# Kernel optimization log

Hardware: AMD Instinct MI355X
Metric: run time of the kernel (lower is better)

## Reference

```python
import jax, jax.numpy as jnp
import numpy as np

B, T, D, HS = 8, 2048, 1024, 64

def setup_inputs() -> dict:
    key = jax.random.key(0)
    ks = jax.random.split(key, 7)
    s = 1.0 / np.sqrt(D)
    return {
        "x": jax.random.normal(ks[0], (B, T, D), dtype=jnp.float32),
        "wq_w": jax.random.normal(ks[1], (HS, D), dtype=jnp.float32) * s,
        "wq_b": jax.random.normal(ks[2], (HS,), dtype=jnp.float32) * 0.01,
        "wk_w": jax.random.normal(ks[3], (HS, D), dtype=jnp.float32) * s,
        "wk_b": jax.random.normal(ks[4], (HS,), dtype=jnp.float32) * 0.01,
        "wv_w": jax.random.normal(ks[5], (HS, D), dtype=jnp.float32) * s,
        "wv_b": jax.random.normal(ks[6], (HS,), dtype=jnp.float32) * 0.01,
    }

def reference(x, wq_w, wq_b, wk_w, wk_b, wv_w, wv_b):
    Tq = x.shape[1]
    q = jnp.einsum('btd,hd->bth', x, wq_w) + wq_b  # [B,T,HS]
    k = jnp.einsum('btd,hd->bth', x, wk_w) + wk_b
    v = jnp.einsum('btd,hd->bth', x, wv_w) + wv_b
    scores = jnp.einsum('bth,bsh->bts', q, k) / jnp.sqrt(jnp.float32(HS))  # [B,T,T]
    causal = jnp.tril(jnp.ones((Tq, Tq), dtype=bool))
    scores = jnp.where(causal, scores, -jnp.inf)
    weight = jax.nn.softmax(scores, axis=-1)
    # dropout p=0.0 -> identity
    out = jnp.einsum('bts,bsh->bth', weight, v)  # [B,T,HS]
    return out
```

## Files before the change

### kernel.cpp

```cpp
#include <hip/hip_runtime.h>

#define DD 1024
#define HSZ 64
#define TT 2048
#define NB 8
#define MM (NB*TT)
#define PART_STRIDE 1040

typedef unsigned short U16;
typedef U16 u16x4 __attribute__((ext_vector_type(4)));
typedef U16 u16x8 __attribute__((ext_vector_type(8)));
typedef float f32x4 __attribute__((ext_vector_type(4)));

__device__ inline U16 f2b(float f) {
    unsigned u = __builtin_bit_cast(unsigned, f);
    u += 0x7FFFu + ((u >> 16) & 1u);
    return (U16)(u >> 16);
}

__device__ inline f32x4 mfma16(u16x8 a, u16x8 b, f32x4 c) {
    return __builtin_amdgcn_mfma_f32_16x16x32_bf16(a, b, c, 0, 0, 0);
}

__device__ inline void gld16(const void* g, void* l) {
    __builtin_amdgcn_global_load_lds(
        (const __attribute__((address_space(1))) void*)g,
        (__attribute__((address_space(3))) void*)l, 16, 0, 0);
}

__global__ __launch_bounds__(256) void wconv_kernel(
    const float* __restrict__ wq, const float* __restrict__ wk,
    const float* __restrict__ wv, U16* __restrict__ wb)
{
    int t = blockIdx.x * 256 + threadIdx.x;
    int n = t >> 8;
    int k0 = (t & 255) * 4;
    const float* src = n < 64 ? wq + (size_t)n * DD
                     : (n < 128 ? wk + (size_t)(n - 64) * DD
                                : wv + (size_t)(n - 128) * DD);
    float4 v = *(const float4*)(src + k0);
    int chunk = k0 >> 6, kc = k0 & 63;
    int byte = (n * 128 + kc * 2) ^ ((n & 7) << 4);
    u16x4 h = { f2b(v.x), f2b(v.y), f2b(v.z), f2b(v.w) };
    *(u16x4*)((char*)wb + (size_t)chunk * 24576 + byte) = h;
}

__global__ __launch_bounds__(512) void qkv_kernel(
    const float* __restrict__ x, const U16* __restrict__ wb,
    const float* __restrict__ wqb, const float* __restrict__ wkb, const float* __restrict__ wvb,
    U16* __restrict__ qb, U16* __restrict__ kb, U16* __restrict__ vt)
{
    __shared__ __attribute__((aligned(16))) U16 Bs[2][12288];
    __shared__ __attribute__((aligned(16))) U16 As[2][2048];

    const int tid = threadIdx.x, lane = tid & 63, w = tid >> 6;
    const int wm = w >> 2, wn = w & 3, g = lane >> 4, c = lane & 15;
    const int m0 = blockIdx.x * 32;

    const int arow = tid >> 4, aseg = tid & 15;
    const float* axp = x + (size_t)(m0 + arow) * DD + aseg * 4;
    const int abyte = (arow * 128 + aseg * 8) ^ ((arow & 7) << 4);

    f32x4 acc[3] = {};
    float4 ar0;

    {
        ar0 = *(const float4*)(axp);
        const char* src = (const char*)wb + tid * 16;
        char* dst = (char*)&Bs[0][0] + tid * 16;
        #pragma unroll
        for (int it = 0; it < 3; ++it) gld16(src + it * 8192, dst + it * 8192);
        u16x4 h = { f2b(ar0.x), f2b(ar0.y), f2b(ar0.z), f2b(ar0.w) };
        *(u16x4*)((char*)&As[0][0] + abyte) = h;
    }
    __syncthreads();

    for (int ch = 0; ch < 16; ++ch) {
        const int cur = ch & 1, nxt = cur ^ 1;
        if (ch < 15) {
            ar0 = *(const float4*)(axp + (ch + 1) * 64);
            const char* src = (const char*)wb + (size_t)(ch + 1) * 24576 + tid * 16;
            char* dst = (char*)&Bs[nxt][0] + tid * 16;
            #pragma unroll
            for (int it = 0; it < 3; ++it) gld16(src + it * 8192, dst + it * 8192);
        }
        #pragma unroll
        for (int ks = 0; ks < 2; ++ks) {
            const int rl = wm * 16 + c;
            u16x8 af = *(const u16x8*)((const char*)&As[cur][0] +
                        ((rl * 128 + ks * 64 + g * 16) ^ ((rl & 7) << 4)));
            #pragma unroll
            for (int nf = 0; nf < 3; ++nf) {
                const int n = wn * 48 + nf * 16 + c;
                u16x8 bf = *(const u16x8*)((const char*)&Bs[cur][0] +
                            ((n * 128 + ks * 64 + g * 16) ^ ((n & 7) << 4)));
                acc[nf] = mfma16(af, bf, acc[nf]);
            }
        }
        if (ch < 15) {
            u16x4 h = { f2b(ar0.x), f2b(ar0.y), f2b(ar0.z), f2b(ar0.w) };
            *(u16x4*)((char*)&As[nxt][0] + abyte) = h;
        }
        __syncthreads();
    }

    #pragma unroll
    for (int nf = 0; nf < 3; ++nf) {
        const int col = wn * 48 + nf * 16 + c;
        const int head = col >> 6, h = col & 63;
        const float bv = head == 0 ? wqb[h] : (head == 1 ? wkb[h] : wvb[h]);
        #pragma unroll
        for (int r = 0; r < 4; ++r) {
            const int row = m0 + wm * 16 + g * 4 + r;
            const float val = acc[nf][r] + bv;
            if (head == 0)      qb[(size_t)row * HSZ + h] = f2b(val * 0.125f);
            else if (head == 1) kb[(size_t)row * HSZ + h] = f2b(val);
            else {
                const int b = row >> 11, tok = row & 2047;
                vt[(((size_t)b * 32 + (tok >> 6)) * 64 + h) * 64 + (tok & 63)] = f2b(val);
            }
        }
    }
}

__global__ __launch_bounds__(256) void attn_kernel(
    const U16* __restrict__ qb, const U16* __restrict__ kb, const U16* __restrict__ vt,
    float* __restrict__ part)
{
    __shared__ __attribute__((aligned(16))) U16 Ps[4][1024];

    const int tid = threadIdx.x, lane = tid & 63, w = tid >> 6;
    const int g = lane >> 4, c = lane & 15;
    const int jid = blockIdx.x * 4 + w;
    const int chunk = jid & 7;
    const int j = (jid >> 3) & 127;
    const int batch = jid >> 10;
    const int a = j >> 4;
    if (chunk > a) return;

    const int q0 = j * 16;
    const size_t base = (size_t)batch * TT;
    const int nt = (j >> 2) + 1;
    const int t0 = chunk * 4;
    const int t_end = (chunk == a) ? nt : t0 + 4;
    char* psw = (char*)&Ps[w][0];

    u16x8 aq[2];
    {
        const U16* qp = qb + (base + q0 + c) * HSZ;
        aq[0] = *(const u16x8*)(qp + g * 8);
        aq[1] = *(const u16x8*)(qp + 32 + g * 8);
    }

    f32x4 acc[4] = {};
    float lsum[4] = {};
    const U16* kbase = kb + base * HSZ + c * HSZ + g * 8;
    const U16* vbase = vt + (size_t)batch * 32 * 4096 + c * 64 + g * 8;

    auto kissue = [&](int t, u16x8 (&kf)[8]) {
        const U16* kp = kbase + t * 64 * HSZ;
        #pragma unroll
        for (int i = 0; i < 8; ++i)
            kf[i] = *(const u16x8*)(kp + (i & 3) * 16 * HSZ + (i >> 2) * 32);
    };

    auto compute = [&](int t, u16x8 (&kf)[8]) {
        u16x8 vf[8];
        const U16* vp = vbase + t * 4096;
        #pragma unroll
        for (int i = 0; i < 8; ++i)
            vf[i] = *(const u16x8*)(vp + (i & 3) * 16 * 64 + (i >> 2) * 32);

        f32x4 s[4] = {};
        #pragma unroll
        for (int i = 0; i < 8; ++i)
            s[i & 3] = mfma16(aq[i >> 2], kf[i], s[i & 3]);

        if (t == nt - 1) {
            #pragma unroll
            for (int nf = 0; nf < 4; ++nf)
                #pragma unroll
                for (int r = 0; r < 4; ++r)
                    if (t * 64 + nf * 16 + c > q0 + g * 4 + r) s[nf][r] = -1e30f;
        }

        #pragma unroll
        for (int nf = 0; nf < 4; ++nf)
            #pragma unroll
            for (int r = 0; r < 4; ++r) {
                const float p = __expf(s[nf][r]);
                lsum[r] += p;
                const int row = g * 4 + r, col = nf * 16 + c;
                *(U16*)(psw + ((row * 128 + col * 2) ^ ((row & 7) << 4))) = f2b(p);
            }
        u16x8 pa[2];
        #pragma unroll
        for (int ks = 0; ks < 2; ++ks)
            pa[ks] = *(const u16x8*)(psw + ((c * 128 + ks * 64 + g * 16) ^ ((c & 7) << 4)));
        #pragma unroll
        for (int i = 0; i < 8; ++i)
            acc[i & 3] = mfma16(pa[i >> 2], vf[i], acc[i & 3]);
    };

    u16x8 kfA[8], kfB[8];
    kissue(t0, kfA);
    for (int t = t0; t < t_end; t += 2) {
        if (t + 1 < t_end) kissue(t + 1, kfB);
        compute(t, kfA);
        if (t + 1 < t_end) {
            if (t + 2 < t_end) kissue(t + 2, kfA);
            compute(t + 1, kfB);
        }
    }

    #pragma unroll
    for (int r = 0; r < 4; ++r) {
        lsum[r] += __shfl_xor(lsum[r], 1);
        lsum[r] += __shfl_xor(lsum[r], 2);
        lsum[r] += __shfl_xor(lsum[r], 4);
        lsum[r] += __shfl_xor(lsum[r], 8);
    }

    const int slot = batch * 576 + (a + 1) * (8 * a + (j & 15)) + chunk;
    float* sp = part + (size_t)slot * PART_STRIDE;
    #pragma unroll
    for (int nf = 0; nf < 4; ++nf)
        #pragma unroll
        for (int r = 0; r < 4; ++r)
            sp[(g * 4 + r) * 64 + nf * 16 + c] = acc[nf][r];
    if (c == 0)
        #pragma unroll
        for (int r = 0; r < 4; ++r)
            sp[1024 + g * 4 + r] = lsum[r];
}

__global__ __launch_bounds__(256) void combine_kernel(
    const float* __restrict__ part, float* __restrict__ out)
{
    const int j = blockIdx.x, batch = blockIdx.y;
    const int a = j >> 4, nc = a + 1;
    const int slot0 = batch * 576 + (a + 1) * (8 * a + (j & 15));
    const int t = threadIdx.x, row = t >> 4, sg = t & 15;
    const float* sp = part + (size_t)slot0 * PART_STRIDE;

    float ox = 0.f, oy = 0.f, oz = 0.f, ow = 0.f, L = 0.f;
    for (int i = 0; i < nc; ++i) {
        L += sp[i * PART_STRIDE + 1024 + row];
        const float4 ov = *(const float4*)&sp[i * PART_STRIDE + row * 64 + sg * 4];
        ox += ov.x; oy += ov.y; oz += ov.z; ow += ov.w;
    }
    const float inv = 1.f / L;
    float4 res = { ox * inv, oy * inv, oz * inv, ow * inv };
    *(float4*)&out[((size_t)batch * TT + j * 16 + row) * HSZ + sg * 4] = res;
}

extern "C" void kernel_launch(void* const* d_in, const int* in_sizes, int n_in,
                              void* d_out, int out_size, void* d_ws, size_t ws_size,
                              hipStream_t stream) {
    const float* x   = (const float*)d_in[0];
    const float* wq  = (const float*)d_in[1];
    const float* wqb = (const float*)d_in[2];
    const float* wk  = (const float*)d_in[3];
    const float* wkb = (const float*)d_in[4];
    const float* wv  = (const float*)d_in[5];
    const float* wvb = (const float*)d_in[6];
    float* out = (float*)d_out;

    U16* wb = (U16*)d_ws;
    U16* qb = wb + 196608;
    U16* kb = qb + (size_t)MM * HSZ;
    U16* vt = kb + (size_t)MM * HSZ;
    float* part = (float*)(vt + (size_t)MM * HSZ);

    wconv_kernel<<<192, 256, 0, stream>>>(wq, wk, wv, wb);
    qkv_kernel<<<512, 512, 0, stream>>>(x, wb, wqb, wkb, wvb, qb, kb, vt);
    attn_kernel<<<2048, 256, 0, stream>>>(qb, kb, vt, part);
    combine_kernel<<<dim3(128, NB), 256, 0, stream>>>(part, out);
}
```

Measured before the change: 179.7 us.

## Share K/V tiles across waves via double-buffered LDS staging in attention

The attention kernel is reorganized so that the four waves of a block handle four consecutive 16-row query groups against the same key chunk. K and V tiles are loaded once per block into swizzled, double-buffered LDS with async global-to-LDS copies, replacing per-wave register loads from global memory. This cuts redundant global/L2 traffic by about 4x for K/V. The cost is a block-wide barrier every tile, extra LDS use and fewer independent waves.

```diff
diff --git a/kernel.cpp b/kernel.cpp
--- a/kernel.cpp
+++ b/kernel.cpp
@@ -127,61 +127,69 @@
     const U16* __restrict__ qb, const U16* __restrict__ kb, const U16* __restrict__ vt,
     float* __restrict__ part)
 {
+    __shared__ __attribute__((aligned(16))) U16 Ks[2][4096];
+    __shared__ __attribute__((aligned(16))) U16 Vs[2][4096];
     __shared__ __attribute__((aligned(16))) U16 Ps[4][1024];
 
     const int tid = threadIdx.x, lane = tid & 63, w = tid >> 6;
-    const int g = lane >> 4, c = lane & 15;
-    const int jid = blockIdx.x * 4 + w;
-    const int chunk = jid & 7;
-    const int j = (jid >> 3) & 127;
-    const int batch = jid >> 10;
-    const int a = j >> 4;
-    if (chunk > a) return;
-
-    const int q0 = j * 16;
-    const size_t base = (size_t)batch * TT;
-    const int nt = (j >> 2) + 1;
-    const int t0 = chunk * 4;
-    const int t_end = (chunk == a) ? nt : t0 + 4;
+    const int gL = lane >> 4, cL = lane & 15;
+    const int g = blockIdx.x >> 3, c = blockIdx.x & 7;
+    const int bb = blockIdx.y;
+    if (c > (g >> 2)) return;
+
+    const int t0 = c * 4;
+    const int t_end = min(t0 + 4, g + 1);
     char* psw = (char*)&Ps[w][0];
 
     u16x8 aq[2];
     {
-        const U16* qp = qb + (base + q0 + c) * HSZ;
-        aq[0] = *(const u16x8*)(qp + g * 8);
-        aq[1] = *(const u16x8*)(qp + 32 + g * 8);
-    }
+        const U16* qp = qb + ((size_t)bb * TT + g * 64 + w * 16 + cL) * HSZ;
+        aq[0] = *(const u16x8*)(qp + gL * 8);
+        aq[1] = *(const u16x8*)(qp + 32 + gL * 8);
+    }
+
+    const U16* kB = kb + (size_t)bb * TT * HSZ;
+    const U16* vB = vt + (size_t)bb * 32 * 4096;
+
+    auto stage = [&](int t, int buf) {
+        #pragma unroll
+        for (int i = 0; i < 2; ++i) {
+            const int b = i * 4096 + tid * 16;
+            const int row = b >> 7, q = b & 127;
+            const int src = q ^ ((row & 7) << 4);
+            gld16((const char*)(kB + (size_t)(t * 64 + row) * HSZ) + src,
+                  (char*)&Ks[buf][0] + b);
+            gld16((const char*)(vB + (size_t)t * 4096 + row * 64) + src,
+                  (char*)&Vs[buf][0] + b);
+        }
+    };
 
     f32x4 acc[4] = {};
     float lsum[4] = {};
-    const U16* kbase = kb + base * HSZ + c * HSZ + g * 8;
-    const U16* vbase = vt + (size_t)batch * 32 * 4096 + c * 64 + g * 8;
-
-    auto kissue = [&](int t, u16x8 (&kf)[8]) {
-        const U16* kp = kbase + t * 64 * HSZ;
-        #pragma unroll
-        for (int i = 0; i < 8; ++i)
-            kf[i] = *(const u16x8*)(kp + (i & 3) * 16 * HSZ + (i >> 2) * 32);
-    };
-
-    auto compute = [&](int t, u16x8 (&kf)[8]) {
-        u16x8 vf[8];
-        const U16* vp = vbase + t * 4096;
-        #pragma unroll
-        for (int i = 0; i < 8; ++i)
-            vf[i] = *(const u16x8*)(vp + (i & 3) * 16 * 64 + (i >> 2) * 32);
+
+    stage(t0, 0);
+    __syncthreads();
+
+    for (int t = t0; t < t_end; ++t) {
+        const int buf = (t - t0) & 1;
+        if (t + 1 < t_end) stage(t + 1, buf ^ 1);
 
         f32x4 s[4] = {};
         #pragma unroll
-        for (int i = 0; i < 8; ++i)
-            s[i & 3] = mfma16(aq[i >> 2], kf[i], s[i & 3]);
-
-        if (t == nt - 1) {
+        for (int ks = 0; ks < 2; ++ks)
+            #pragma unroll
+            for (int nf = 0; nf < 4; ++nf) {
+                u16x8 kf = *(const u16x8*)((const char*)&Ks[buf][0] +
+                            ((nf * 16 + cL) * 128 + ((ks * 64 + gL * 16) ^ ((cL & 7) << 4))));
+                s[nf] = mfma16(aq[ks], kf, s[nf]);
+            }
+
+        if (t == g) {
             #pragma unroll
             for (int nf = 0; nf < 4; ++nf)
                 #pragma unroll
                 for (int r = 0; r < 4; ++r)
-                    if (t * 64 + nf * 16 + c > q0 + g * 4 + r) s[nf][r] = -1e30f;
+                    if (nf * 16 + cL > w * 16 + gL * 4 + r) s[nf][r] = -1e30f;
         }
 
         #pragma unroll
@@ -190,27 +198,24 @@
             for (int r = 0; r < 4; ++r) {
                 const float p = __expf(s[nf][r]);
                 lsum[r] += p;
-                const int row = g * 4 + r, col = nf * 16 + c;
+                const int row = gL * 4 + r, col = nf * 16 + cL;
                 *(U16*)(psw + ((row * 128 + col * 2) ^ ((row & 7) << 4))) = f2b(p);
             }
         u16x8 pa[2];
         #pragma unroll
         for (int ks = 0; ks < 2; ++ks)
-            pa[ks] = *(const u16x8*)(psw + ((c * 128 + ks * 64 + g * 16) ^ ((c & 7) << 4)));
-        #pragma unroll
-        for (int i = 0; i < 8; ++i)
-            acc[i & 3] = mfma16(pa[i >> 2], vf[i], acc[i & 3]);
-    };
-
-    u16x8 kfA[8], kfB[8];
-    kissue(t0, kfA);
-    for (int t = t0; t < t_end; t += 2) {
-        if (t + 1 < t_end) kissue(t + 1, kfB);
-        compute(t, kfA);
-        if (t + 1 < t_end) {
-            if (t + 2 < t_end) kissue(t + 2, kfA);
-            compute(t + 1, kfB);
-        }
+            pa[ks] = *(const u16x8*)(psw + ((cL * 128 + ks * 64 + gL * 16) ^ ((cL & 7) << 4)));
+
+        #pragma unroll
+        for (int ks = 0; ks < 2; ++ks)
+            #pragma unroll
+            for (int nf = 0; nf < 4; ++nf) {
+                u16x8 vf = *(const u16x8*)((const char*)&Vs[buf][0] +
+                            ((nf * 16 + cL) * 128 + ((ks * 64 + gL * 16) ^ ((cL & 7) << 4))));
+                acc[nf] = mfma16(pa[ks], vf, acc[nf]);
+            }
+
+        __syncthreads();
     }
 
     #pragma unroll
@@ -221,17 +226,18 @@
         lsum[r] += __shfl_xor(lsum[r], 8);
     }
 
-    const int slot = batch * 576 + (a + 1) * (8 * a + (j & 15)) + chunk;
+    const int j = 4 * g + w, a = g >> 2;
+    const int slot = bb * 576 + (a + 1) * (8 * a + (j & 15)) + c;
     float* sp = part + (size_t)slot * PART_STRIDE;
     #pragma unroll
     for (int nf = 0; nf < 4; ++nf)
         #pragma unroll
         for (int r = 0; r < 4; ++r)
-            sp[(g * 4 + r) * 64 + nf * 16 + c] = acc[nf][r];
-    if (c == 0)
+            sp[(gL * 4 + r) * 64 + nf * 16 + cL] = acc[nf][r];
+    if (cL == 0)
         #pragma unroll
         for (int r = 0; r < 4; ++r)
-            sp[1024 + g * 4 + r] = lsum[r];
+            sp[1024 + gL * 4 + r] = lsum[r];
 }
 
 __global__ __launch_bounds__(256) void combine_kernel(
@@ -274,6 +280,6 @@
 
     wconv_kernel<<<192, 256, 0, stream>>>(wq, wk, wv, wb);
     qkv_kernel<<<512, 512, 0, stream>>>(x, wb, wqb, wkb, wvb, qb, kb, vt);
-    attn_kernel<<<2048, 256, 0, stream>>>(qb, kb, vt, part);
+    attn_kernel<<<dim3(256, NB), 256, 0, stream>>>(qb, kb, vt, part);
     combine_kernel<<<dim3(128, NB), 256, 0, stream>>>(part, out);
 }
```

After: 146.3 us. 1.23x faster.
